# Optimization experiments

Hardware: AMD Instinct MI355X
Metric: run time of the kernel (lower is better)

The kernel has to match this reference:

```python
import jax, jax.numpy as jnp
import numpy as np

QMIN, QMAX = 0.0, 255.0  # uint8 affine quantization range


def setup_inputs() -> dict:
    key = jax.random.key(0)
    ks = jax.random.split(key, 7)
    B, S, IN, OUT = 4, 2048, 4096, 4096
    x = jax.random.normal(ks[0], (B, S, IN), dtype=jnp.float32)
    weight_q = jax.random.randint(ks[1], (OUT, IN), 0, 255, dtype=jnp.int32)
    weight_scales = jax.random.uniform(ks[2], (OUT,), dtype=jnp.float32) * 0.01 + 1e-4
    weight_zero_points = jax.random.randint(ks[3], (OUT,), 0, 255, dtype=jnp.int32)
    act_scales = jax.random.uniform(ks[4], (1,), dtype=jnp.float32) * 0.05 + 1e-3
    act_zero_points = jnp.full((1,), 128, dtype=jnp.int32)
    bias = jax.random.normal(ks[5], (OUT,), dtype=jnp.float32)
    return {
        "x": x,
        "weight_q": weight_q,
        "weight_scales": weight_scales,
        "weight_zero_points": weight_zero_points,
        "act_scales": act_scales,
        "act_zero_points": act_zero_points,
        "bias": bias,
    }


def reference(x, weight_q, weight_scales, weight_zero_points, act_scales, act_zero_points, bias):
    # quantize_from_qparams on activations (per-tensor affine, uint8 range)
    a_zp = act_zero_points.astype(jnp.float32)
    x_q = jnp.clip(jnp.round(x / act_scales) + a_zp, QMIN, QMAX)
    # linear_on_quantized_data: dequantize both operands, fused matmul + bias
    x_deq = (x_q - a_zp) * act_scales  # [B, S, IN]
    w_deq = (weight_q.astype(jnp.float32) - weight_zero_points.astype(jnp.float32)[:, None]) \
            * weight_scales[:, None]  # [OUT, IN], per-output-channel scale/zp
    out = jnp.einsum("bsi,oi->bso", x_deq, w_deq) + bias  # [B, S, OUT]
    return out
```

## Files before the change

kernel.cpp:

```cpp
#include <hip/hip_runtime.h>
#include <hip/hip_bf16.h>

using int32x4 = __attribute__((ext_vector_type(4))) int;

#define BM 128
#define BN 128
#define BKQ 128

__device__ __forceinline__ void load_lds16(const void* g, void* l) {
    __builtin_amdgcn_global_load_lds(
        (const __attribute__((address_space(1))) unsigned int*)g,
        (__attribute__((address_space(3))) unsigned int*)l, 16, 0, 0);
}

__global__ __launch_bounds__(256) void quant_rows(
    const float* __restrict__ x, const float* __restrict__ act_scale,
    const int* __restrict__ act_zp, char* __restrict__ xs,
    int* __restrict__ rowsum, int K)
{
    __shared__ int wsum[4];
    const int row = blockIdx.x;
    const float s = act_scale[0];
    const int zp = act_zp[0];
    const float4* __restrict__ xr = (const float4*)(x + (size_t)row * K);
    char4* __restrict__ xo = (char4*)(xs + (size_t)row * K);
    const int nv = K >> 2;
    int sum = 0;
    for (int i = threadIdx.x; i < nv; i += 256) {
        float4 v = xr[i];
        int q0 = min(max((int)rintf(v.x / s) + zp, 0), 255) - zp;
        int q1 = min(max((int)rintf(v.y / s) + zp, 0), 255) - zp;
        int q2 = min(max((int)rintf(v.z / s) + zp, 0), 255) - zp;
        int q3 = min(max((int)rintf(v.w / s) + zp, 0), 255) - zp;
        sum += q0 + q1 + q2 + q3;
        char4 c;
        c.x = (char)q0; c.y = (char)q1; c.z = (char)q2; c.w = (char)q3;
        xo[i] = c;
    }
    for (int off = 32; off > 0; off >>= 1) sum += __shfl_down(sum, off, 64);
    if ((threadIdx.x & 63) == 0) wsum[threadIdx.x >> 6] = sum;
    __syncthreads();
    if (threadIdx.x == 0) rowsum[row] = wsum[0] + wsum[1] + wsum[2] + wsum[3];
}

__global__ __launch_bounds__(256) void wconv(
    const int4* __restrict__ wq, char4* __restrict__ wsq, long n4)
{
    long i = (long)blockIdx.x * 256 + threadIdx.x;
    if (i >= n4) return;
    int4 v = wq[i];
    char4 c;
    c.x = (char)(v.x - 128); c.y = (char)(v.y - 128);
    c.z = (char)(v.z - 128); c.w = (char)(v.w - 128);
    wsq[i] = c;
}

__global__ __launch_bounds__(256) void mkscales(
    const float* __restrict__ wscale, const int* __restrict__ wzp,
    const float* __restrict__ act_scale, float* __restrict__ alpha,
    float* __restrict__ beta, int N)
{
    int n = blockIdx.x * 256 + threadIdx.x;
    if (n >= N) return;
    float a = act_scale[0] * wscale[n];
    alpha[n] = a;
    beta[n] = a * (float)(128 - wzp[n]);
}

__global__ __launch_bounds__(256, 4) void gemm_i8(
    const char* __restrict__ Aq, const char* __restrict__ Bq,
    const int* __restrict__ rowsum, const float* __restrict__ alpha,
    const float* __restrict__ beta, const float* __restrict__ bias,
    float* __restrict__ C, int M, int N, int K)
{
    __shared__ __align__(16) char As[BM * BKQ];
    __shared__ __align__(16) char Bs[BN * BKQ];

    const int tid  = threadIdx.x;
    const int wave = tid >> 6;
    const int lane = tid & 63;

    const int n0 = blockIdx.x * BN;
    const int m0 = blockIdx.y * BM;

    const int wm = (wave & 1) * 64;
    const int wn = (wave >> 1) * 64;

    const int srow = wave * 8 + (lane >> 3);
    const int scol = ((lane & 7) ^ (lane >> 3)) * 16;
    const char* ag = Aq + (size_t)(m0 + srow) * K + scol;
    const char* bg = Bq + (size_t)(n0 + srow) * K + scol;
    const size_t band = (size_t)32 * K;

    char* lA = As + wave * 1024;
    char* lB = Bs + wave * 1024;

    int32x4 acc[4][4] = {};

    const int r  = lane & 15;
    const int q  = lane >> 4;
    const int rx = r & 7;

    for (int k0 = 0; k0 < K; k0 += BKQ) {
        __syncthreads();
#pragma unroll
        for (int u = 0; u < 4; u++) {
            load_lds16(ag + u * band, lA + u * 4096);
            load_lds16(bg + u * band, lB + u * 4096);
        }
        ag += BKQ;
        bg += BKQ;
        __syncthreads();

#pragma unroll
        for (int kb = 0; kb < 2; kb++) {
            int32x4 af[4], bf[4];
#pragma unroll
            for (int i = 0; i < 4; i++)
                af[i] = *(const int32x4*)(As + (wm + i * 16 + r) * 128
                                             + (((kb * 4 + q) ^ rx) * 16));
#pragma unroll
            for (int j = 0; j < 4; j++)
                bf[j] = *(const int32x4*)(Bs + (wn + j * 16 + r) * 128
                                             + (((kb * 4 + q) ^ rx) * 16));
#pragma unroll
            for (int i = 0; i < 4; i++)
#pragma unroll
                for (int j = 0; j < 4; j++)
                    acc[i][j] = __builtin_amdgcn_mfma_i32_16x16x64_i8(
                        af[i], bf[j], acc[i][j], 0, 0, 0);
        }
    }

    const int r4  = (lane >> 4) * 4;
    const int cil = lane & 15;
#pragma unroll
    for (int j = 0; j < 4; j++) {
        const int col = n0 + wn + j * 16 + cil;
        const float al = alpha[col];
        const float be = beta[col];
        const float bi = bias[col];
#pragma unroll
        for (int i = 0; i < 4; i++) {
            const int rowb = m0 + wm + i * 16 + r4;
#pragma unroll
            for (int t = 0; t < 4; t++) {
                const int row = rowb + t;
                C[(size_t)row * N + col] =
                    al * (float)acc[i][j][t] + be * (float)rowsum[row] + bi;
            }
        }
    }
}

extern "C" void kernel_launch(void* const* d_in, const int* in_sizes, int n_in,
                              void* d_out, int out_size, void* d_ws, size_t ws_size,
                              hipStream_t stream) {
    const float* x      = (const float*)d_in[0];
    const int*   wq     = (const int*)d_in[1];
    const float* wscale = (const float*)d_in[2];
    const int*   wzp    = (const int*)d_in[3];
    const float* ascale = (const float*)d_in[4];
    const int*   azp    = (const int*)d_in[5];
    const float* bias   = (const float*)d_in[6];
    float* out = (float*)d_out;

    const int N = in_sizes[2];
    const int K = in_sizes[1] / N;
    const int M = in_sizes[0] / K;

    char* ws     = (char*)d_ws;
    char* xs     = ws;
    char* wsq    = ws + (size_t)M * K;
    int*  rowsum = (int*)(wsq + (size_t)N * K);
    float* alpha = (float*)((char*)rowsum + (size_t)M * 4);
    float* beta  = (float*)((char*)alpha + (size_t)N * 4);

    quant_rows<<<M, 256, 0, stream>>>(x, ascale, azp, xs, rowsum, K);

    long n4 = (long)N * K / 4;
    wconv<<<(int)((n4 + 255) / 256), 256, 0, stream>>>(
        (const int4*)wq, (char4*)wsq, n4);

    mkscales<<<(N + 255) / 256, 256, 0, stream>>>(wscale, wzp, ascale, alpha, beta, N);

    dim3 grid(N / BN, M / BM);
    gemm_i8<<<grid, 256, 0, stream>>>(xs, wsq, rowsum, alpha, beta, bias, out, M, N, K);
}
```

Baseline: 409.6 us.

## Rewrite int8 GEMM with 256x256 tiles, double-buffered LDS pipeline and XCD remap

The GEMM now uses 512-thread blocks on 256x256 output tiles. Global-to-LDS loads go into double buffers and are interleaved with MFMA phases, gated by vmcnt waits and raw barriers. Workgroup IDs are remapped so adjacent tiles land on the same XCD for L2 reuse, and MFMA issue priority is raised with setprio. The larger tile cuts global traffic per FLOP and the pipeline hides load latency. In exchange it uses 128 KB of LDS and more accumulator registers, which lowers occupancy, and the hand-placed waitcnt gating depends on exact load counts.

```diff
diff --git a/kernel.cpp b/kernel.cpp
--- a/kernel.cpp
+++ b/kernel.cpp
@@ -3,9 +3,11 @@
 
 using int32x4 = __attribute__((ext_vector_type(4))) int;
 
-#define BM 128
-#define BN 128
-#define BKQ 128
+#define BM 256
+#define BN 256
+#define BKB 128
+
+#define GATE(n) asm volatile("s_waitcnt vmcnt(" #n ")" ::: "memory")
 
 __device__ __forceinline__ void load_lds16(const void* g, void* l) {
     __builtin_amdgcn_global_load_lds(
@@ -67,87 +69,141 @@
     beta[n] = a * (float)(128 - wzp[n]);
 }
 
-__global__ __launch_bounds__(256, 4) void gemm_i8(
+__global__ __launch_bounds__(512, 2) void gemm_i8(
     const char* __restrict__ Aq, const char* __restrict__ Bq,
     const int* __restrict__ rowsum, const float* __restrict__ alpha,
     const float* __restrict__ beta, const float* __restrict__ bias,
     float* __restrict__ C, int M, int N, int K)
 {
-    __shared__ __align__(16) char As[BM * BKQ];
-    __shared__ __align__(16) char Bs[BN * BKQ];
-
-    const int tid  = threadIdx.x;
-    const int wave = tid >> 6;
-    const int lane = tid & 63;
-
-    const int n0 = blockIdx.x * BN;
-    const int m0 = blockIdx.y * BM;
-
-    const int wm = (wave & 1) * 64;
-    const int wn = (wave >> 1) * 64;
-
-    const int srow = wave * 8 + (lane >> 3);
-    const int scol = ((lane & 7) ^ (lane >> 3)) * 16;
-    const char* ag = Aq + (size_t)(m0 + srow) * K + scol;
-    const char* bg = Bq + (size_t)(n0 + srow) * K + scol;
-    const size_t band = (size_t)32 * K;
-
-    char* lA = As + wave * 1024;
-    char* lB = Bs + wave * 1024;
-
-    int32x4 acc[4][4] = {};
-
-    const int r  = lane & 15;
-    const int q  = lane >> 4;
-    const int rx = r & 7;
-
-    for (int k0 = 0; k0 < K; k0 += BKQ) {
-        __syncthreads();
-#pragma unroll
-        for (int u = 0; u < 4; u++) {
-            load_lds16(ag + u * band, lA + u * 4096);
-            load_lds16(bg + u * band, lB + u * 4096);
+    __shared__ __align__(16) char As[2][BM * BKB];
+    __shared__ __align__(16) char Bs[2][BN * BKB];
+
+    const int tid = threadIdx.x;
+    const int w   = tid >> 6;
+    const int l   = tid & 63;
+
+    const int nwg = gridDim.x;
+    const int nbx = N / BN;
+    const int orig = blockIdx.x;
+    const int xcd = orig & 7;
+    const int rest = orig >> 3;
+    const int qq = nwg >> 3, rr = nwg & 7;
+    const int wg = (xcd < rr ? xcd * (qq + 1) : rr * (qq + 1) + (xcd - rr) * qq)
+                   + rest;
+    const int n0 = (wg % nbx) * BN;
+    const int m0 = (wg / nbx) * BM;
+
+    const int wm = (w & 1) * 128;
+    const int wn = (w >> 1) * 64;
+
+    const int lr8 = l >> 3;
+    const int csw = (((l & 7) ^ (lr8 & 7)) << 4);
+    const int rB0 = w * 16;
+    const int rA2 = (w < 4) ? (w * 16) : (128 + (w - 4) * 16);
+
+    const char* sB0 = Bq + (size_t)(n0 + rB0 + lr8) * K + csw;
+    const char* sB1 = sB0 + (size_t)128 * K;
+    const char* sA2 = Aq + (size_t)(m0 + rA2 + lr8) * K + csw;
+    const char* sA3 = sA2 + (size_t)64 * K;
+    const size_t k8 = (size_t)8 * K;
+
+    const int oB0 = rB0 * BKB;
+    const int oB1 = oB0 + 128 * BKB;
+    const int oA2 = rA2 * BKB;
+    const int oA3 = oA2 + 64 * BKB;
+
+    const int r   = l & 15;
+    const int qk  = l >> 4;
+    const int rx  = r & 7;
+    const int rof = r * BKB;
+    const int ck0 = ((qk ^ rx) << 4);
+    const int ck1 = (((4 + qk) ^ rx) << 4);
+
+    int32x4 acc[8][4] = {};
+    const int NT = K / BKB;
+
+    load_lds16(sB0,      Bs[0] + oB0);
+    load_lds16(sB0 + k8, Bs[0] + oB0 + 1024);
+    load_lds16(sB1,      Bs[0] + oB1);
+    load_lds16(sB1 + k8, Bs[0] + oB1 + 1024);
+    load_lds16(sA2,      As[0] + oA2);
+    load_lds16(sA2 + k8, As[0] + oA2 + 1024);
+    load_lds16(sA3,      As[0] + oA3);
+    load_lds16(sA3 + k8, As[0] + oA3 + 1024);
+    sB0 += BKB; sB1 += BKB; sA2 += BKB; sA3 += BKB;
+
+    int s = 0;
+    for (int T = 0; T < NT; ++T) {
+        const char* cA = As[s];
+        const char* cB = Bs[s];
+        char* nA = As[s ^ 1];
+        char* nB = Bs[s ^ 1];
+        const bool stage = (T + 1 < NT);
+        int32x4 bf[4][2];
+#pragma unroll
+        for (int p = 0; p < 4; ++p) {
+            if (p == 0) { GATE(2); }
+            if (p == 2) { if (stage) { GATE(4); } else { GATE(0); } }
+            __builtin_amdgcn_s_barrier();
+
+            int32x4 af[2][2];
+            const char* ab = cA + (wm + p * 32) * BKB + rof;
+            af[0][0] = *(const int32x4*)(ab + ck0);
+            af[0][1] = *(const int32x4*)(ab + ck1);
+            af[1][0] = *(const int32x4*)(ab + 2048 + ck0);
+            af[1][1] = *(const int32x4*)(ab + 2048 + ck1);
+            if (p == 0) {
+                const char* bb = cB + wn * BKB + rof;
+#pragma unroll
+                for (int j = 0; j < 4; ++j) {
+                    bf[j][0] = *(const int32x4*)(bb + j * 2048 + ck0);
+                    bf[j][1] = *(const int32x4*)(bb + j * 2048 + ck1);
+                }
+            }
+            if (stage) {
+                if (p == 0) { load_lds16(sB0, nB + oB0);
+                              load_lds16(sB0 + k8, nB + oB0 + 1024); }
+                if (p == 1) { load_lds16(sB1, nB + oB1);
+                              load_lds16(sB1 + k8, nB + oB1 + 1024); }
+                if (p == 2) { load_lds16(sA2, nA + oA2);
+                              load_lds16(sA2 + k8, nA + oA2 + 1024); }
+                if (p == 3) { load_lds16(sA3, nA + oA3);
+                              load_lds16(sA3 + k8, nA + oA3 + 1024); }
+            }
+            asm volatile("s_waitcnt lgkmcnt(0)" ::: "memory");
+            __builtin_amdgcn_sched_barrier(0);
+            __builtin_amdgcn_s_setprio(1);
+#pragma unroll
+            for (int i = 0; i < 2; ++i)
+#pragma unroll
+                for (int j = 0; j < 4; ++j) {
+                    acc[p * 2 + i][j] = __builtin_amdgcn_mfma_i32_16x16x64_i8(
+                        af[i][0], bf[j][0], acc[p * 2 + i][j], 0, 0, 0);
+                    acc[p * 2 + i][j] = __builtin_amdgcn_mfma_i32_16x16x64_i8(
+                        af[i][1], bf[j][1], acc[p * 2 + i][j], 0, 0, 0);
+                }
+            __builtin_amdgcn_s_setprio(0);
         }
-        ag += BKQ;
-        bg += BKQ;
-        __syncthreads();
-
-#pragma unroll
-        for (int kb = 0; kb < 2; kb++) {
-            int32x4 af[4], bf[4];
-#pragma unroll
-            for (int i = 0; i < 4; i++)
-                af[i] = *(const int32x4*)(As + (wm + i * 16 + r) * 128
-                                             + (((kb * 4 + q) ^ rx) * 16));
-#pragma unroll
-            for (int j = 0; j < 4; j++)
-                bf[j] = *(const int32x4*)(Bs + (wn + j * 16 + r) * 128
-                                             + (((kb * 4 + q) ^ rx) * 16));
-#pragma unroll
-            for (int i = 0; i < 4; i++)
-#pragma unroll
-                for (int j = 0; j < 4; j++)
-                    acc[i][j] = __builtin_amdgcn_mfma_i32_16x16x64_i8(
-                        af[i], bf[j], acc[i][j], 0, 0, 0);
-        }
+        sB0 += BKB; sB1 += BKB; sA2 += BKB; sA3 += BKB;
+        s ^= 1;
     }
 
-    const int r4  = (lane >> 4) * 4;
-    const int cil = lane & 15;
-#pragma unroll
-    for (int j = 0; j < 4; j++) {
+    const int r4  = qk * 4;
+    const int cil = r;
+#pragma unroll
+    for (int j = 0; j < 4; ++j) {
         const int col = n0 + wn + j * 16 + cil;
         const float al = alpha[col];
         const float be = beta[col];
         const float bi = bias[col];
 #pragma unroll
-        for (int i = 0; i < 4; i++) {
-            const int rowb = m0 + wm + i * 16 + r4;
-#pragma unroll
-            for (int t = 0; t < 4; t++) {
+        for (int mi = 0; mi < 8; ++mi) {
+            const int rowb = m0 + wm + mi * 16 + r4;
+#pragma unroll
+            for (int t = 0; t < 4; ++t) {
                 const int row = rowb + t;
                 C[(size_t)row * N + col] =
-                    al * (float)acc[i][j][t] + be * (float)rowsum[row] + bi;
+                    al * (float)acc[mi][j][t] + be * (float)rowsum[row] + bi;
             }
         }
     }
@@ -184,6 +240,6 @@
 
     mkscales<<<(N + 255) / 256, 256, 0, stream>>>(wscale, wzp, ascale, alpha, beta, N);
 
-    dim3 grid(N / BN, M / BM);
-    gemm_i8<<<grid, 256, 0, stream>>>(xs, wsq, rowsum, alpha, beta, bias, out, M, N, K);
-}
+    dim3 grid((M / BM) * (N / BN));
+    gemm_i8<<<grid, 512, 0, stream>>>(xs, wsq, rowsum, alpha, beta, bias, out, M, N, K);
+}
```

After: 426.0 us. 1.04x slower.

## Switch int8 GEMM to 32x32x32 MFMA and merge prep kernels

Applied to the files above, without the earlier changes.

The GEMM inner loop now uses 32x32x32 i8 MFMA instructions on 2x2 tiles per wave instead of 16x16x64 on 4x4 tiles, which halves the LDS fragment loads per k-step. The activation quantization and weight conversion kernels are merged into one launch. The per-column scale computation moves into the GEMM epilogue, removing the separate mkscales kernel and its buffers. The epilogue store pattern changes to match the 32x32 output layout, which may alter write coalescing.

```diff
diff --git a/kernel.cpp b/kernel.cpp
--- a/kernel.cpp
+++ b/kernel.cpp
@@ -1,7 +1,8 @@
 #include <hip/hip_runtime.h>
 #include <hip/hip_bf16.h>
 
-using int32x4 = __attribute__((ext_vector_type(4))) int;
+using int32x4  = __attribute__((ext_vector_type(4))) int;
+using int32x16 = __attribute__((ext_vector_type(16))) int;
 
 #define BM 128
 #define BN 128
@@ -13,65 +14,53 @@
         (__attribute__((address_space(3))) unsigned int*)l, 16, 0, 0);
 }
 
-__global__ __launch_bounds__(256) void quant_rows(
+__global__ __launch_bounds__(256) void prep(
     const float* __restrict__ x, const float* __restrict__ act_scale,
     const int* __restrict__ act_zp, char* __restrict__ xs,
-    int* __restrict__ rowsum, int K)
-{
-    __shared__ int wsum[4];
-    const int row = blockIdx.x;
-    const float s = act_scale[0];
-    const int zp = act_zp[0];
-    const float4* __restrict__ xr = (const float4*)(x + (size_t)row * K);
-    char4* __restrict__ xo = (char4*)(xs + (size_t)row * K);
-    const int nv = K >> 2;
-    int sum = 0;
-    for (int i = threadIdx.x; i < nv; i += 256) {
-        float4 v = xr[i];
-        int q0 = min(max((int)rintf(v.x / s) + zp, 0), 255) - zp;
-        int q1 = min(max((int)rintf(v.y / s) + zp, 0), 255) - zp;
-        int q2 = min(max((int)rintf(v.z / s) + zp, 0), 255) - zp;
-        int q3 = min(max((int)rintf(v.w / s) + zp, 0), 255) - zp;
-        sum += q0 + q1 + q2 + q3;
-        char4 c;
-        c.x = (char)q0; c.y = (char)q1; c.z = (char)q2; c.w = (char)q3;
-        xo[i] = c;
-    }
-    for (int off = 32; off > 0; off >>= 1) sum += __shfl_down(sum, off, 64);
-    if ((threadIdx.x & 63) == 0) wsum[threadIdx.x >> 6] = sum;
-    __syncthreads();
-    if (threadIdx.x == 0) rowsum[row] = wsum[0] + wsum[1] + wsum[2] + wsum[3];
-}
-
-__global__ __launch_bounds__(256) void wconv(
+    int* __restrict__ rowsum, int K, int M,
     const int4* __restrict__ wq, char4* __restrict__ wsq, long n4)
 {
-    long i = (long)blockIdx.x * 256 + threadIdx.x;
-    if (i >= n4) return;
-    int4 v = wq[i];
-    char4 c;
-    c.x = (char)(v.x - 128); c.y = (char)(v.y - 128);
-    c.z = (char)(v.z - 128); c.w = (char)(v.w - 128);
-    wsq[i] = c;
-}
-
-__global__ __launch_bounds__(256) void mkscales(
-    const float* __restrict__ wscale, const int* __restrict__ wzp,
-    const float* __restrict__ act_scale, float* __restrict__ alpha,
-    float* __restrict__ beta, int N)
-{
-    int n = blockIdx.x * 256 + threadIdx.x;
-    if (n >= N) return;
-    float a = act_scale[0] * wscale[n];
-    alpha[n] = a;
-    beta[n] = a * (float)(128 - wzp[n]);
+    if (blockIdx.x < (unsigned)M) {
+        __shared__ int wsum[4];
+        const int row = blockIdx.x;
+        const float s = act_scale[0];
+        const int zp = act_zp[0];
+        const float4* __restrict__ xr = (const float4*)(x + (size_t)row * K);
+        char4* __restrict__ xo = (char4*)(xs + (size_t)row * K);
+        const int nv = K >> 2;
+        int sum = 0;
+        for (int i = threadIdx.x; i < nv; i += 256) {
+            float4 v = xr[i];
+            int q0 = min(max((int)rintf(v.x / s) + zp, 0), 255) - zp;
+            int q1 = min(max((int)rintf(v.y / s) + zp, 0), 255) - zp;
+            int q2 = min(max((int)rintf(v.z / s) + zp, 0), 255) - zp;
+            int q3 = min(max((int)rintf(v.w / s) + zp, 0), 255) - zp;
+            sum += q0 + q1 + q2 + q3;
+            char4 c;
+            c.x = (char)q0; c.y = (char)q1; c.z = (char)q2; c.w = (char)q3;
+            xo[i] = c;
+        }
+        for (int off = 32; off > 0; off >>= 1) sum += __shfl_down(sum, off, 64);
+        if ((threadIdx.x & 63) == 0) wsum[threadIdx.x >> 6] = sum;
+        __syncthreads();
+        if (threadIdx.x == 0) rowsum[row] = wsum[0] + wsum[1] + wsum[2] + wsum[3];
+    } else {
+        long i = (long)(blockIdx.x - M) * 256 + threadIdx.x;
+        if (i >= n4) return;
+        int4 v = wq[i];
+        char4 c;
+        c.x = (char)(v.x - 128); c.y = (char)(v.y - 128);
+        c.z = (char)(v.z - 128); c.w = (char)(v.w - 128);
+        wsq[i] = c;
+    }
 }
 
 __global__ __launch_bounds__(256, 4) void gemm_i8(
     const char* __restrict__ Aq, const char* __restrict__ Bq,
-    const int* __restrict__ rowsum, const float* __restrict__ alpha,
-    const float* __restrict__ beta, const float* __restrict__ bias,
-    float* __restrict__ C, int M, int N, int K)
+    const int* __restrict__ rowsum, const float* __restrict__ wscale,
+    const int* __restrict__ wzp, const float* __restrict__ ascale,
+    const float* __restrict__ bias, float* __restrict__ C,
+    int M, int N, int K)
 {
     __shared__ __align__(16) char As[BM * BKQ];
     __shared__ __align__(16) char Bs[BN * BKQ];
@@ -95,11 +84,11 @@
     char* lA = As + wave * 1024;
     char* lB = Bs + wave * 1024;
 
-    int32x4 acc[4][4] = {};
+    int32x16 acc[2][2] = {};
 
-    const int r  = lane & 15;
-    const int q  = lane >> 4;
-    const int rx = r & 7;
+    const int rA = lane & 31;
+    const int hf = lane >> 5;
+    const int rx = rA & 7;
 
     for (int k0 = 0; k0 < K; k0 += BKQ) {
         __syncthreads();
@@ -113,41 +102,33 @@
         __syncthreads();
 
 #pragma unroll
-        for (int kb = 0; kb < 2; kb++) {
-            int32x4 af[4], bf[4];
-#pragma unroll
-            for (int i = 0; i < 4; i++)
-                af[i] = *(const int32x4*)(As + (wm + i * 16 + r) * 128
-                                             + (((kb * 4 + q) ^ rx) * 16));
-#pragma unroll
-            for (int j = 0; j < 4; j++)
-                bf[j] = *(const int32x4*)(Bs + (wn + j * 16 + r) * 128
-                                             + (((kb * 4 + q) ^ rx) * 16));
-#pragma unroll
-            for (int i = 0; i < 4; i++)
-#pragma unroll
-                for (int j = 0; j < 4; j++)
-                    acc[i][j] = __builtin_amdgcn_mfma_i32_16x16x64_i8(
-                        af[i], bf[j], acc[i][j], 0, 0, 0);
+        for (int ss = 0; ss < 4; ss++) {
+            const int pc = (((ss * 2 + hf) ^ rx) << 4);
+            int32x4 a0 = *(const int32x4*)(As + (wm + rA) * 128 + pc);
+            int32x4 a1 = *(const int32x4*)(As + (wm + 32 + rA) * 128 + pc);
+            int32x4 b0 = *(const int32x4*)(Bs + (wn + rA) * 128 + pc);
+            int32x4 b1 = *(const int32x4*)(Bs + (wn + 32 + rA) * 128 + pc);
+            acc[0][0] = __builtin_amdgcn_mfma_i32_32x32x32_i8(a0, b0, acc[0][0], 0, 0, 0);
+            acc[0][1] = __builtin_amdgcn_mfma_i32_32x32x32_i8(a0, b1, acc[0][1], 0, 0, 0);
+            acc[1][0] = __builtin_amdgcn_mfma_i32_32x32x32_i8(a1, b0, acc[1][0], 0, 0, 0);
+            acc[1][1] = __builtin_amdgcn_mfma_i32_32x32x32_i8(a1, b1, acc[1][1], 0, 0, 0);
         }
     }
 
-    const int r4  = (lane >> 4) * 4;
-    const int cil = lane & 15;
+    const float as = ascale[0];
 #pragma unroll
-    for (int j = 0; j < 4; j++) {
-        const int col = n0 + wn + j * 16 + cil;
-        const float al = alpha[col];
-        const float be = beta[col];
+    for (int nt = 0; nt < 2; nt++) {
+        const int col = n0 + wn + nt * 32 + rA;
+        const float al = as * wscale[col];
+        const float be = al * (float)(128 - wzp[col]);
         const float bi = bias[col];
 #pragma unroll
-        for (int i = 0; i < 4; i++) {
-            const int rowb = m0 + wm + i * 16 + r4;
+        for (int mt = 0; mt < 2; mt++) {
 #pragma unroll
-            for (int t = 0; t < 4; t++) {
-                const int row = rowb + t;
+            for (int t = 0; t < 16; t++) {
+                const int row = m0 + wm + mt * 32 + (t & 3) + 8 * (t >> 2) + 4 * hf;
                 C[(size_t)row * N + col] =
-                    al * (float)acc[i][j][t] + be * (float)rowsum[row] + bi;
+                    al * (float)acc[mt][nt][t] + be * (float)rowsum[row] + bi;
             }
         }
     }
@@ -173,17 +154,13 @@
     char* xs     = ws;
     char* wsq    = ws + (size_t)M * K;
     int*  rowsum = (int*)(wsq + (size_t)N * K);
-    float* alpha = (float*)((char*)rowsum + (size_t)M * 4);
-    float* beta  = (float*)((char*)alpha + (size_t)N * 4);
-
-    quant_rows<<<M, 256, 0, stream>>>(x, ascale, azp, xs, rowsum, K);
 
     long n4 = (long)N * K / 4;
-    wconv<<<(int)((n4 + 255) / 256), 256, 0, stream>>>(
-        (const int4*)wq, (char4*)wsq, n4);
-
-    mkscales<<<(N + 255) / 256, 256, 0, stream>>>(wscale, wzp, ascale, alpha, beta, N);
+    int wblocks = (int)((n4 + 255) / 256);
+    prep<<<M + wblocks, 256, 0, stream>>>(
+        x, ascale, azp, xs, rowsum, K, M, (const int4*)wq, (char4*)wsq, n4);
 
     dim3 grid(N / BN, M / BM);
-    gemm_i8<<<grid, 256, 0, stream>>>(xs, wsq, rowsum, alpha, beta, bias, out, M, N, K);
+    gemm_i8<<<grid, 256, 0, stream>>>(
+        xs, wsq, rowsum, wscale, wzp, ascale, bias, out, M, N, K);
 }
```

Measured after the change: 436.7 us. +6.6%, slower.
